# Kernel optimization log

Measured on AMD Instinct MI355X. Metric: run time of the kernel, lower is better.

The kernel has to match this reference:

```python
import jax, jax.numpy as jnp
import numpy as np

LN_EPS = 1e-5


def _ln(h, g, b):
    mu = h.mean(-1, keepdims=True)
    var = ((h - mu) ** 2).mean(-1, keepdims=True)
    return (h - mu) / jnp.sqrt(var + LN_EPS) * g + b


def setup_inputs() -> dict:
    key = jax.random.key(0)
    ks = jax.random.split(key, 12)
    B, T, Cin, C, D, M = 16, 1024, 512, 1024, 256, 1024
    s = 0.02
    inp = {
        "x": jax.random.normal(ks[0], (B, T, Cin), jnp.float32),
        "masks": jnp.ones((B, T), jnp.float32),
        "W1": jax.random.normal(ks[1], (Cin, C), jnp.float32) * s,
        "g1": jnp.ones((C,), jnp.float32), "b1": jnp.zeros((C,), jnp.float32),
        "W2": jax.random.normal(ks[2], (C, C), jnp.float32) * s,
        "g2": jnp.ones((C,), jnp.float32), "b2": jnp.zeros((C,), jnp.float32),
        "W3": jax.random.normal(ks[3], (C, C), jnp.float32) * s,
        "g3": jnp.ones((C,), jnp.float32), "b3": jnp.zeros((C,), jnp.float32),
        "W4": jax.random.normal(ks[4], (C, C), jnp.float32) * s,
        "g4": jnp.ones((C,), jnp.float32), "b4": jnp.zeros((C,), jnp.float32),
        "W5": jax.random.normal(ks[5], (C, D), jnp.float32) * s,
        "b5": jnp.zeros((D,), jnp.float32),
        # Dirichlet(alpha=100) rows, as in the torch init: rows live on the simplex
        "embedding": jax.random.dirichlet(ks[6], jnp.full((D,), 100.0, jnp.float32), (M,)).astype(jnp.float32),
    }
    return inp


def reference(x, masks, W1, g1, b1, W2, g2, b2, W3, g3, b3, W4, g4, b4, W5, b5, embedding):
    h = jax.nn.relu(_ln(x @ W1, g1, b1))
    h = jax.nn.relu(_ln(h @ W2, g2, b2))
    h = jax.nn.relu(_ln(h @ W3, g3, b3))
    h = jax.nn.relu(_ln(h @ W4, g4, b4))
    z = h @ W5 + b5                              # [B, T, D]
    p = jax.nn.log_softmax(z, axis=-1)           # log-prob features

    B, T, D = p.shape
    p_flat = jax.lax.stop_gradient(p.reshape(-1, D))   # x.detach() in torch
    ep = jnp.exp(p_flat)                               # [N, D]
    # KL(exp(p) || e_m) summed over D, for all codes m:
    #   sum_d exp(p)*(p - log(e_m)) = rowsum(exp(p)*p) - exp(p) @ log(E)^T
    div = (ep * p_flat).sum(-1, keepdims=True) - ep @ jnp.log(embedding).T  # [N, M]
    idx = jnp.argmin(div, axis=-1)                     # [N]
    quant = jax.lax.stop_gradient(embedding[idx].reshape(B, T, D))

    # commitment loss: masked KL(exp(p) || quant.detach())
    kl = (jnp.exp(p) * (p - jnp.log(quant))).sum(-1)   # [B, T]
    loss = 0.25 * (kl * masks).mean(0).sum()

    # straight-through estimator
    q = p + jax.lax.stop_gradient(quant - p)
    return z, q, loss
```

## Files before the change

### kernel.cpp

```cpp
#include <hip/hip_runtime.h>
#include <hip/hip_bf16.h>
#include <stdint.h>

typedef __attribute__((ext_vector_type(4))) float f32x4;
typedef __attribute__((ext_vector_type(8))) __bf16 bf16x8;
typedef __attribute__((ext_vector_type(4))) __bf16 bf16x4;

#define LN_EPS 1e-5f

__device__ __forceinline__ void gload_lds16(const void* g, void* l) {
  __builtin_amdgcn_global_load_lds(
      (__attribute__((address_space(1))) void*)(uintptr_t)g,
      (__attribute__((address_space(3))) void*)(uint32_t)(uintptr_t)l,
      16, 0, 0);
}

__device__ __forceinline__ f32x4 mfma16(bf16x8 a, bf16x8 b, f32x4 c) {
  return __builtin_amdgcn_mfma_f32_16x16x32_bf16(a, b, c, 0, 0, 0);
}

__global__ __launch_bounds__(256) void k_cvt_bf16(const float* __restrict__ x,
                                                  __bf16* __restrict__ o) {
  int i = (blockIdx.x * 256 + threadIdx.x) * 8;
  f32x4 a = *(const f32x4*)(x + i);
  f32x4 b = *(const f32x4*)(x + i + 4);
  bf16x8 v;
#pragma unroll
  for (int j = 0; j < 4; ++j) { v[j] = (__bf16)a[j]; v[j + 4] = (__bf16)b[j]; }
  *(bf16x8*)(o + i) = v;
}

__global__ void k_transpose(const float* __restrict__ W, __bf16* __restrict__ Wt,
                            int K, int N) {
  __shared__ float t[32][33];
  int nt = blockIdx.x * 32, kt = blockIdx.y * 32;
  int tx = threadIdx.x, ty = threadIdx.y;
  t[ty][tx] = W[(size_t)(kt + ty) * N + nt + tx];
  __syncthreads();
  Wt[(size_t)(nt + ty) * K + kt + tx] = (__bf16)t[tx][ty];
}

__global__ void k_transpose3(const float* __restrict__ Wa, const float* __restrict__ Wb,
                             const float* __restrict__ Wc, __bf16* __restrict__ Ta,
                             __bf16* __restrict__ Tb, __bf16* __restrict__ Tc) {
  __shared__ float t[32][33];
  const float* W = blockIdx.z == 0 ? Wa : (blockIdx.z == 1 ? Wb : Wc);
  __bf16* T = blockIdx.z == 0 ? Ta : (blockIdx.z == 1 ? Tb : Tc);
  int nt = blockIdx.x * 32, kt = blockIdx.y * 32;
  int tx = threadIdx.x, ty = threadIdx.y;
  t[ty][tx] = W[(size_t)(kt + ty) * 1024 + nt + tx];
  __syncthreads();
  T[(size_t)(nt + ty) * 1024 + kt + tx] = (__bf16)t[tx][ty];
}

__global__ __launch_bounds__(256) void k_logE(const float* __restrict__ e,
                                              __bf16* __restrict__ o) {
  int i = blockIdx.x * 256 + threadIdx.x;
  o[i] = (__bf16)logf(e[i] * 256.0f);
}

__global__ __launch_bounds__(512, 2) void k_gemm256(
    const __bf16* __restrict__ A, const __bf16* __restrict__ Bt,
    __bf16* __restrict__ O, int N, int K) {
  __shared__ char lds[131072];
  const int tid = threadIdx.x;
  const int lane = tid & 63;
  const int wid = tid >> 6;
  const int wm = wid >> 2;
  const int wn = wid & 3;
  const int swz = ((blockIdx.x & 7) << 5) | (blockIdx.x >> 3);
  const int bm0 = (swz & 63) * 256;
  const int bn0 = (swz >> 6) * 256;
  const int NT = K >> 6;

  const int slin = tid * 16;
  const int lrow = slin >> 7;
  const int scol = (slin & 127) ^ ((lrow & 7) << 4);
  const char* Ab = (const char*)A;
  const char* Bb = (const char*)Bt;
  const uint32_t rs = (uint32_t)K * 2;

  const int klo = (lane >> 4) * 16;
  const int sw = (lane & 7) << 4;
  const uint32_t kx0 = (uint32_t)(klo ^ sw);
  const uint32_t kx1 = (uint32_t)((64 + klo) ^ sw);
  const uint32_t abase = (uint32_t)(wm * 128 + (lane & 15)) * 128;
  const uint32_t bbase = (uint32_t)(wn * 64 + (lane & 15)) * 128;

  f32x4 acc[8][4];
#pragma unroll
  for (int i = 0; i < 8; ++i)
#pragma unroll
    for (int j = 0; j < 4; ++j) acc[i][j] = 0.0f;

#define LDSA(buf) (lds + (buf)*32768)
#define LDSB(buf) (lds + 65536 + (buf)*32768)
#define STAGE_A(t, h)                                                              \
  {                                                                                \
    const char* src = Ab + (size_t)(bm0 + (h)*128 + lrow) * rs + ((t) << 7) + scol;\
    char* dst = LDSA((t)&1) + (h)*16384 + slin;                                    \
    gload_lds16(src, dst);                                                         \
    gload_lds16(src + (size_t)64 * rs, dst + 8192);                                \
  }
#define STAGE_B(t, h)                                                              \
  {                                                                                \
    const char* src = Bb + (size_t)(bn0 + (h)*128 + lrow) * rs + ((t) << 7) + scol;\
    char* dst = LDSB((t)&1) + (h)*16384 + slin;                                    \
    gload_lds16(src, dst);                                                         \
    gload_lds16(src + (size_t)64 * rs, dst + 8192);                                \
  }

  STAGE_A(0, 0); STAGE_A(0, 1); STAGE_B(0, 0); STAGE_B(0, 1);
  STAGE_B(1, 0); STAGE_B(1, 1);
  asm volatile("s_waitcnt vmcnt(4)" ::: "memory");
  __builtin_amdgcn_s_barrier();
  asm volatile("" ::: "memory");

  for (int t = 0; t < NT; ++t) {
    const char* Acur = LDSA(t & 1);
    const char* Bcur = LDSB(t & 1);
    bf16x8 bF[4][2];
#pragma unroll
    for (int p = 0; p < 4; ++p) {
      const uint32_t ar = abase + (uint32_t)(2 * p) * 2048;
      bf16x8 a00 = *(const bf16x8*)(Acur + ar + kx0);
      bf16x8 a01 = *(const bf16x8*)(Acur + ar + kx1);
      bf16x8 a10 = *(const bf16x8*)(Acur + ar + 2048 + kx0);
      bf16x8 a11 = *(const bf16x8*)(Acur + ar + 2048 + kx1);
      if (p == 0) {
#pragma unroll
        for (int ni = 0; ni < 4; ++ni) {
          bF[ni][0] = *(const bf16x8*)(Bcur + bbase + ni * 2048 + kx0);
          bF[ni][1] = *(const bf16x8*)(Bcur + bbase + ni * 2048 + kx1);
        }
      }
      if (p == 0 && t + 1 < NT) STAGE_A(t + 1, 0);
      if (p == 1) {
        if (t + 1 < NT) STAGE_A(t + 1, 1);
        if (t + 2 < NT) STAGE_B(t + 2, 0);
      }
      if (p == 2 && t + 2 < NT) STAGE_B(t + 2, 1);

      asm volatile("" ::: "memory");
      __builtin_amdgcn_s_barrier();
      asm volatile("" ::: "memory");
      __builtin_amdgcn_s_setprio(1);
#pragma unroll
      for (int ni = 0; ni < 4; ++ni) {
        acc[2 * p][ni] = mfma16(a00, bF[ni][0], acc[2 * p][ni]);
        acc[2 * p][ni] = mfma16(a01, bF[ni][1], acc[2 * p][ni]);
        acc[2 * p + 1][ni] = mfma16(a10, bF[ni][0], acc[2 * p + 1][ni]);
        acc[2 * p + 1][ni] = mfma16(a11, bF[ni][1], acc[2 * p + 1][ni]);
      }
      __builtin_amdgcn_s_setprio(0);
      if (p == 3) asm volatile("s_waitcnt vmcnt(4)" ::: "memory");
      asm volatile("" ::: "memory");
      __builtin_amdgcn_s_barrier();
      asm volatile("" ::: "memory");
    }
  }
#undef STAGE_A
#undef STAGE_B
#undef LDSA
#undef LDSB

  const int r0 = (lane >> 4) * 4;
  const int cc = lane & 15;
#pragma unroll
  for (int mi = 0; mi < 8; ++mi) {
#pragma unroll
    for (int ni = 0; ni < 4; ++ni) {
      int r = bm0 + wm * 128 + mi * 16 + r0;
      int c = bn0 + wn * 64 + ni * 16 + cc;
#pragma unroll
      for (int j = 0; j < 4; ++j)
        O[(size_t)(r + j) * N + c] = (__bf16)acc[mi][ni][j];
    }
  }
}

__global__ __launch_bounds__(256) void k_ln_relu(__bf16* __restrict__ h,
                                                 const float* __restrict__ g,
                                                 const float* __restrict__ b) {
  int lane = threadIdx.x & 63;
  int row = blockIdx.x * 4 + (threadIdx.x >> 6);
  __bf16* rp = h + (size_t)row * 1024;
  bf16x8 v0 = *(const bf16x8*)(rp + lane * 8);
  bf16x8 v1 = *(const bf16x8*)(rp + 512 + lane * 8);
  float f0[8], f1[8];
  float s = 0.f, sq = 0.f;
#pragma unroll
  for (int j = 0; j < 8; ++j) {
    f0[j] = (float)v0[j]; f1[j] = (float)v1[j];
    s += f0[j] + f1[j];
    sq += f0[j] * f0[j] + f1[j] * f1[j];
  }
#pragma unroll
  for (int d = 1; d < 64; d <<= 1) { s += __shfl_xor(s, d); sq += __shfl_xor(sq, d); }
  float mu = s * (1.0f / 1024.0f);
  float var = sq * (1.0f / 1024.0f) - mu * mu;
  float rstd = rsqrtf(var + LN_EPS);
  const f32x4* gv = (const f32x4*)g;
  const f32x4* bv = (const f32x4*)b;
  f32x4 ga0 = gv[lane * 2], ga1 = gv[lane * 2 + 1];
  f32x4 gb0 = gv[128 + lane * 2], gb1 = gv[128 + lane * 2 + 1];
  f32x4 ba0 = bv[lane * 2], ba1 = bv[lane * 2 + 1];
  f32x4 bb0 = bv[128 + lane * 2], bb1 = bv[128 + lane * 2 + 1];
  bf16x8 o0, o1;
#pragma unroll
  for (int j = 0; j < 4; ++j) {
    float t0 = (f0[j] - mu) * rstd * ga0[j] + ba0[j];
    float t1 = (f0[j + 4] - mu) * rstd * ga1[j] + ba1[j];
    float t2 = (f1[j] - mu) * rstd * gb0[j] + bb0[j];
    float t3 = (f1[j + 4] - mu) * rstd * gb1[j] + bb1[j];
    o0[j] = (__bf16)fmaxf(t0, 0.f);
    o0[j + 4] = (__bf16)fmaxf(t1, 0.f);
    o1[j] = (__bf16)fmaxf(t2, 0.f);
    o1[j + 4] = (__bf16)fmaxf(t3, 0.f);
  }
  *(bf16x8*)(rp + lane * 8) = o0;
  *(bf16x8*)(rp + 512 + lane * 8) = o1;
}

__global__ __launch_bounds__(256) void k_gemm_sm(
    const __bf16* __restrict__ A, const __bf16* __restrict__ Bt,
    const float* __restrict__ bias, float* __restrict__ z,
    __bf16* __restrict__ ep, float* __restrict__ sm) {
  const int K = 1024;
  __shared__ char lds[40960];
  char* ldsA = lds;
  char* ldsB = lds + 8192;
  const int tid = threadIdx.x;
  const int lane = tid & 63;
  const int wn = tid >> 6;
  const int bm0 = blockIdx.x * 64;
  const char* Ab = (const char*)A;
  const char* Bb = (const char*)Bt;
  const uint32_t rs = (uint32_t)K * 2;

  const int cc = lane & 15;
  uint32_t ra[2][4], rb[2][4];
  {
    const int sww = (lane & 7) << 4;
    const int gk = lane & 48;
#pragma unroll
    for (int kk = 0; kk < 2; ++kk) {
#pragma unroll
      for (int i = 0; i < 4; ++i) {
        uint32_t kb = (uint32_t)((kk * 64 + gk) ^ sww);
        ra[kk][i] = (uint32_t)(i * 16 + cc) * 128 + kb;
        rb[kk][i] = (uint32_t)(wn * 64 + i * 16 + cc) * 128 + kb;
      }
    }
  }

  f32x4 acc[4][4];
#pragma unroll
  for (int i = 0; i < 4; ++i)
#pragma unroll
    for (int j = 0; j < 4; ++j) acc[i][j] = 0.0f;

  for (int k0 = 0; k0 < K; k0 += 64) {
    __syncthreads();
#pragma unroll
    for (int i = 0; i < 2; ++i) {
      int lin = i * 4096 + tid * 16;
      int row = lin >> 7;
      int col = (lin & 127) ^ ((row & 7) << 4);
      gload_lds16(Ab + (size_t)(bm0 + row) * rs + k0 * 2 + col, ldsA + lin);
    }
#pragma unroll
    for (int i = 0; i < 8; ++i) {
      int lin = i * 4096 + tid * 16;
      int row = lin >> 7;
      int col = (lin & 127) ^ ((row & 7) << 4);
      gload_lds16(Bb + (size_t)row * rs + k0 * 2 + col, ldsB + lin);
    }
    __syncthreads();
#pragma unroll
    for (int kk = 0; kk < 2; ++kk) {
      bf16x8 af[4], bfv[4];
#pragma unroll
      for (int i = 0; i < 4; ++i) af[i] = *(const bf16x8*)(ldsA + ra[kk][i]);
#pragma unroll
      for (int i = 0; i < 4; ++i) bfv[i] = *(const bf16x8*)(ldsB + rb[kk][i]);
#pragma unroll
      for (int mi = 0; mi < 4; ++mi)
#pragma unroll
        for (int ni = 0; ni < 4; ++ni)
          acc[mi][ni] = mfma16(af[mi], bfv[ni], acc[mi][ni]);
    }
  }

  __syncthreads();
  float* stm = (float*)lds;
  float* sts = (float*)(lds + 1024);
  float* rowm = (float*)(lds + 2048);
  float* rows_ = (float*)(lds + 2304);

  const int r0 = (lane >> 4) * 4;
  float bvv[4];
#pragma unroll
  for (int ni = 0; ni < 4; ++ni) bvv[ni] = bias[wn * 64 + ni * 16 + cc];

  float zv[4][4];
#pragma unroll
  for (int mi = 0; mi < 4; ++mi) {
#pragma unroll
    for (int j = 0; j < 4; ++j) {
      float m = -3.4e38f;
#pragma unroll
      for (int ni = 0; ni < 4; ++ni) {
        zv[mi][ni] = acc[mi][ni][j] + bvv[ni];
        m = fmaxf(m, zv[mi][ni]);
      }
#pragma unroll
      for (int d = 1; d < 16; d <<= 1) m = fmaxf(m, __shfl_xor(m, d));
      if (cc == 0) stm[wn * 64 + mi * 16 + r0 + j] = m;
    }
  }
  __syncthreads();
  if (tid < 64) {
    float m = fmaxf(fmaxf(stm[tid], stm[64 + tid]), fmaxf(stm[128 + tid], stm[192 + tid]));
    rowm[tid] = m;
  }
  __syncthreads();
#pragma unroll
  for (int mi = 0; mi < 4; ++mi) {
#pragma unroll
    for (int j = 0; j < 4; ++j) {
      int r = mi * 16 + r0 + j;
      float m = rowm[r];
      float s = 0.f;
#pragma unroll
      for (int ni = 0; ni < 4; ++ni) s += expf(acc[mi][ni][j] + bvv[ni] - m);
#pragma unroll
      for (int d = 1; d < 16; d <<= 1) s += __shfl_xor(s, d);
      if (cc == 0) sts[wn * 64 + r] = s;
    }
  }
  __syncthreads();
  if (tid < 64) {
    float s = sts[tid] + sts[64 + tid] + sts[128 + tid] + sts[192 + tid];
    rows_[tid] = s;
    sm[bm0 + tid] = rowm[tid] + logf(s);
  }
  __syncthreads();
#pragma unroll
  for (int mi = 0; mi < 4; ++mi) {
#pragma unroll
    for (int j = 0; j < 4; ++j) {
      int r = mi * 16 + r0 + j;
      float m = rowm[r];
      float inv = 1.0f / rows_[r];
      float* zp = z + (size_t)(bm0 + r) * 256;
      __bf16* epp = ep + (size_t)(bm0 + r) * 256;
#pragma unroll
      for (int ni = 0; ni < 4; ++ni) {
        int c = wn * 64 + ni * 16 + cc;
        float zz = acc[mi][ni][j] + bvv[ni];
        zp[c] = zz;
        epp[c] = (__bf16)(expf(zz - m) * inv);
      }
    }
  }
}

__global__ __launch_bounds__(256) void k_gemm_div(
    const __bf16* __restrict__ A, const __bf16* __restrict__ Bt,
    float* __restrict__ part_val, int* __restrict__ part_idx, int N, int K) {
  __shared__ char lds[32768];
  char* ldsA = lds;
  char* ldsB = lds + 16384;
  const int tid = threadIdx.x;
  const int lane = tid & 63;
  const int wid = tid >> 6;
  const int wm = wid >> 1, wn = wid & 1;
  const int bm0 = blockIdx.x * 128;
  const int bn0 = blockIdx.y * 128;

  const int slin = tid * 16;
  const int srow = slin >> 7;
  const int scol = (slin & 127) ^ ((srow & 7) << 4);

  const char* Ab = (const char*)A;
  const char* Bb = (const char*)Bt;
  const uint32_t rs = (uint32_t)K * 2;

  uint32_t ra[2][4], rb[2][4];
  {
    const int sw = (lane & 7) << 4;
    const int gk = lane & 48;
#pragma unroll
    for (int kk = 0; kk < 2; ++kk) {
#pragma unroll
      for (int i = 0; i < 4; ++i) {
        uint32_t kb = (uint32_t)((kk * 64 + gk) ^ sw);
        ra[kk][i] = (uint32_t)(wm * 64 + i * 16 + (lane & 15)) * 128 + kb;
        rb[kk][i] = (uint32_t)(wn * 64 + i * 16 + (lane & 15)) * 128 + kb;
      }
    }
  }

  f32x4 acc[4][4];
#pragma unroll
  for (int i = 0; i < 4; ++i)
#pragma unroll
    for (int j = 0; j < 4; ++j) acc[i][j] = 0.0f;

  for (int k0 = 0; k0 < K; k0 += 64) {
    __syncthreads();
    const uint32_t kbyte = (uint32_t)k0 * 2 + (uint32_t)scol;
#pragma unroll
    for (int i = 0; i < 4; ++i) {
      int row = i * 32 + srow;
      gload_lds16(Ab + (size_t)(bm0 + row) * rs + kbyte, ldsA + i * 4096 + slin);
    }
#pragma unroll
    for (int i = 0; i < 4; ++i) {
      int row = i * 32 + srow;
      gload_lds16(Bb + (size_t)(bn0 + row) * rs + kbyte, ldsB + i * 4096 + slin);
    }
    __syncthreads();
#pragma unroll
    for (int kk = 0; kk < 2; ++kk) {
      bf16x8 af[4], bfv[4];
#pragma unroll
      for (int i = 0; i < 4; ++i) af[i] = *(const bf16x8*)(ldsA + ra[kk][i]);
#pragma unroll
      for (int i = 0; i < 4; ++i) bfv[i] = *(const bf16x8*)(ldsB + rb[kk][i]);
#pragma unroll
      for (int mi = 0; mi < 4; ++mi)
#pragma unroll
        for (int ni = 0; ni < 4; ++ni)
          acc[mi][ni] = mfma16(af[mi], bfv[ni], acc[mi][ni]);
    }
  }

  const int r0 = (lane >> 4) * 4;
  const int cc = lane & 15;
  const int nch = N >> 6;
#pragma unroll
  for (int mi = 0; mi < 4; ++mi) {
#pragma unroll
    for (int j = 0; j < 4; ++j) {
      float v = acc[mi][0][j];
      int c = cc;
#pragma unroll
      for (int ni = 1; ni < 4; ++ni) {
        float v2 = acc[mi][ni][j];
        int c2 = ni * 16 + cc;
        if (v2 > v) { v = v2; c = c2; }
      }
#pragma unroll
      for (int d = 1; d < 16; d <<= 1) {
        float ov = __shfl_xor(v, d);
        int oc = __shfl_xor(c, d);
        if (ov > v || (ov == v && oc < c)) { v = ov; c = oc; }
      }
      if (cc == 0) {
        int r = bm0 + wm * 64 + mi * 16 + r0 + j;
        int chunk = (bn0 >> 6) + wn;
        part_val[r * nch + chunk] = v;
        part_idx[r * nch + chunk] = bn0 + wn * 64 + c;
      }
    }
  }
}

__global__ __launch_bounds__(256) void k_final(
    const float* __restrict__ part_val, const int* __restrict__ part_idx,
    const float* __restrict__ z, const float* __restrict__ sm,
    const float* __restrict__ emb, const float* __restrict__ masks,
    float* __restrict__ q, float* __restrict__ blockloss) {
  __shared__ float ls[4];
  int lane = threadIdx.x & 63;
  int w = threadIdx.x >> 6;
  int row = blockIdx.x * 4 + w;
  float v = -3.4e38f;
  int c = 0x7fffffff;
  if (lane < 16) { v = part_val[row * 16 + lane]; c = part_idx[row * 16 + lane]; }
#pragma unroll
  for (int d = 1; d < 16; d <<= 1) {
    float ov = __shfl_xor(v, d);
    int oc = __shfl_xor(c, d);
    if (ov > v || (ov == v && oc < c)) { v = ov; c = oc; }
  }
  int code = __shfl(c, 0);
  f32x4 ev = ((const f32x4*)(emb + (size_t)code * 256))[lane];
  ((f32x4*)(q + (size_t)row * 256))[lane] = ev;
  f32x4 zv = ((const f32x4*)(z + (size_t)row * 256))[lane];
  float smr = sm[row];
  float kl = 0.f;
#pragma unroll
  for (int j = 0; j < 4; ++j) {
    float pj = zv[j] - smr;
    kl += expf(pj) * (pj - logf(ev[j]));
  }
#pragma unroll
  for (int d = 1; d < 64; d <<= 1) kl += __shfl_xor(kl, d);
  if (lane == 0) ls[w] = kl * masks[row];
  __syncthreads();
  if (threadIdx.x == 0) blockloss[blockIdx.x] = ls[0] + ls[1] + ls[2] + ls[3];
}

__global__ __launch_bounds__(256) void k_loss_reduce(const float* __restrict__ bl,
                                                     float* __restrict__ out) {
  __shared__ float s[256];
  float a = 0.f;
#pragma unroll
  for (int i = 0; i < 16; ++i) a += bl[threadIdx.x + i * 256];
  s[threadIdx.x] = a;
  __syncthreads();
  for (int st = 128; st > 0; st >>= 1) {
    if (threadIdx.x < st) s[threadIdx.x] += s[threadIdx.x + st];
    __syncthreads();
  }
  if (threadIdx.x == 0) out[0] = s[0] * (0.25f / 16.0f);
}

extern "C" void kernel_launch(void* const* d_in, const int* in_sizes, int n_in,
                              void* d_out, int out_size, void* d_ws, size_t ws_size,
                              hipStream_t stream) {
  const float* x = (const float*)d_in[0];
  const float* masks = (const float*)d_in[1];
  const float* W1 = (const float*)d_in[2];
  const float* g1 = (const float*)d_in[3];
  const float* b1 = (const float*)d_in[4];
  const float* W2 = (const float*)d_in[5];
  const float* g2 = (const float*)d_in[6];
  const float* b2 = (const float*)d_in[7];
  const float* W3 = (const float*)d_in[8];
  const float* g3 = (const float*)d_in[9];
  const float* b3 = (const float*)d_in[10];
  const float* W4 = (const float*)d_in[11];
  const float* g4 = (const float*)d_in[12];
  const float* b4 = (const float*)d_in[13];
  const float* W5 = (const float*)d_in[14];
  const float* b5 = (const float*)d_in[15];
  const float* emb = (const float*)d_in[16];

  const int M = 16384;
  char* ws = (char*)d_ws;
  __bf16* bufA = (__bf16*)(ws);
  __bf16* bufB = (__bf16*)(ws + (32ull << 20));
  __bf16* W1t = (__bf16*)(ws + (64ull << 20));
  __bf16* W2t = (__bf16*)(ws + (65ull << 20));
  __bf16* W3t = (__bf16*)(ws + (67ull << 20));
  __bf16* W4t = (__bf16*)(ws + (69ull << 20));
  __bf16* W5t = (__bf16*)(ws + (71ull << 20));
  __bf16* logE = (__bf16*)(ws + (72ull << 20));
  float* part_val = (float*)(ws + (73ull << 20));
  int* part_idx = (int*)(ws + (74ull << 20));
  float* blockloss = (float*)(ws + (75ull << 20));
  float* sm = (float*)(ws + (76ull << 20));
  __bf16* ep = (__bf16*)(ws + (16ull << 20));

  float* z = (float*)d_out;
  float* q = z + (size_t)M * 256;
  float* lossp = z + 2ull * M * 256;

  dim3 tb32(32, 32);
  k_cvt_bf16<<<4096, 256, 0, stream>>>(x, bufB);
  k_transpose<<<dim3(32, 16), tb32, 0, stream>>>(W1, W1t, 512, 1024);
  k_transpose3<<<dim3(32, 32, 3), tb32, 0, stream>>>(W2, W3, W4, W2t, W3t, W4t);
  k_transpose<<<dim3(8, 32), tb32, 0, stream>>>(W5, W5t, 1024, 256);
  k_logE<<<1024, 256, 0, stream>>>(emb, logE);

  k_gemm256<<<256, 512, 0, stream>>>(bufB, W1t, bufA, 1024, 512);
  k_ln_relu<<<4096, 256, 0, stream>>>(bufA, g1, b1);
  k_gemm256<<<256, 512, 0, stream>>>(bufA, W2t, bufB, 1024, 1024);
  k_ln_relu<<<4096, 256, 0, stream>>>(bufB, g2, b2);
  k_gemm256<<<256, 512, 0, stream>>>(bufB, W3t, bufA, 1024, 1024);
  k_ln_relu<<<4096, 256, 0, stream>>>(bufA, g3, b3);
  k_gemm256<<<256, 512, 0, stream>>>(bufA, W4t, bufB, 1024, 1024);
  k_ln_relu<<<4096, 256, 0, stream>>>(bufB, g4, b4);
  k_gemm_sm<<<256, 256, 0, stream>>>(bufB, W5t, b5, z, ep, sm);
  k_gemm_div<<<dim3(128, 8), 256, 0, stream>>>(ep, logE, part_val, part_idx, 1024, 256);
  k_final<<<4096, 256, 0, stream>>>(part_val, part_idx, z, sm, emb, masks, q, blockloss);
  k_loss_reduce<<<1, 256, 0, stream>>>(blockloss, lossp);
}
```

Before: 281.4 us.

## Restructure GEMM main loop into two half-phases and drop block swizzle

Rewrites the k_gemm256 inner loop from four quarter-phases with a barrier around each into two half-phases. Each half loads A fragments for four M-subtiles and runs 32 MFMAs, with sched_barriers replacing memory clobbers. Global-to-LDS staging is regrouped: all of next A at loop start, all of B two tiles ahead after the mid barrier. It also replaces the XCD-aware block swizzle with a plain 2D grid, which may change L2 locality across XCDs, and drops a temporary array in the softmax epilogue.

```diff
diff --git a/kernel.cpp b/kernel.cpp
--- a/kernel.cpp
+++ b/kernel.cpp
@@ -68,9 +68,8 @@
   const int wid = tid >> 6;
   const int wm = wid >> 2;
   const int wn = wid & 3;
-  const int swz = ((blockIdx.x & 7) << 5) | (blockIdx.x >> 3);
-  const int bm0 = (swz & 63) * 256;
-  const int bn0 = (swz >> 6) * 256;
+  const int bm0 = blockIdx.x * 256;
+  const int bn0 = blockIdx.y * 256;
   const int NT = K >> 6;
 
   const int slin = tid * 16;
@@ -112,51 +111,63 @@
 
   STAGE_A(0, 0); STAGE_A(0, 1); STAGE_B(0, 0); STAGE_B(0, 1);
   STAGE_B(1, 0); STAGE_B(1, 1);
-  asm volatile("s_waitcnt vmcnt(4)" ::: "memory");
+  asm volatile("s_waitcnt vmcnt(4)");
   __builtin_amdgcn_s_barrier();
-  asm volatile("" ::: "memory");
+  __builtin_amdgcn_sched_barrier(0);
 
   for (int t = 0; t < NT; ++t) {
     const char* Acur = LDSA(t & 1);
     const char* Bcur = LDSB(t & 1);
+
+    if (t + 1 < NT) { STAGE_A(t + 1, 0); STAGE_A(t + 1, 1); }
     bf16x8 bF[4][2];
 #pragma unroll
-    for (int p = 0; p < 4; ++p) {
-      const uint32_t ar = abase + (uint32_t)(2 * p) * 2048;
-      bf16x8 a00 = *(const bf16x8*)(Acur + ar + kx0);
-      bf16x8 a01 = *(const bf16x8*)(Acur + ar + kx1);
-      bf16x8 a10 = *(const bf16x8*)(Acur + ar + 2048 + kx0);
-      bf16x8 a11 = *(const bf16x8*)(Acur + ar + 2048 + kx1);
-      if (p == 0) {
+    for (int ni = 0; ni < 4; ++ni) {
+      bF[ni][0] = *(const bf16x8*)(Bcur + bbase + ni * 2048 + kx0);
+      bF[ni][1] = *(const bf16x8*)(Bcur + bbase + ni * 2048 + kx1);
+    }
+    {
+      bf16x8 aF[4][2];
+#pragma unroll
+      for (int mi = 0; mi < 4; ++mi) {
+        aF[mi][0] = *(const bf16x8*)(Acur + abase + mi * 2048 + kx0);
+        aF[mi][1] = *(const bf16x8*)(Acur + abase + mi * 2048 + kx1);
+      }
+      __builtin_amdgcn_s_setprio(1);
+#pragma unroll
+      for (int mi = 0; mi < 4; ++mi)
 #pragma unroll
         for (int ni = 0; ni < 4; ++ni) {
-          bF[ni][0] = *(const bf16x8*)(Bcur + bbase + ni * 2048 + kx0);
-          bF[ni][1] = *(const bf16x8*)(Bcur + bbase + ni * 2048 + kx1);
+          acc[mi][ni] = mfma16(aF[mi][0], bF[ni][0], acc[mi][ni]);
+          acc[mi][ni] = mfma16(aF[mi][1], bF[ni][1], acc[mi][ni]);
         }
-      }
-      if (p == 0 && t + 1 < NT) STAGE_A(t + 1, 0);
-      if (p == 1) {
-        if (t + 1 < NT) STAGE_A(t + 1, 1);
-        if (t + 2 < NT) STAGE_B(t + 2, 0);
-      }
-      if (p == 2 && t + 2 < NT) STAGE_B(t + 2, 1);
-
-      asm volatile("" ::: "memory");
+      __builtin_amdgcn_s_setprio(0);
+    }
+    __builtin_amdgcn_s_barrier();
+    __builtin_amdgcn_sched_barrier(0);
+
+    if (t + 2 < NT) { STAGE_B(t + 2, 0); STAGE_B(t + 2, 1); }
+    {
+      bf16x8 aF[4][2];
+#pragma unroll
+      for (int mi = 0; mi < 4; ++mi) {
+        aF[mi][0] = *(const bf16x8*)(Acur + abase + (mi + 4) * 2048 + kx0);
+        aF[mi][1] = *(const bf16x8*)(Acur + abase + (mi + 4) * 2048 + kx1);
+      }
+      __builtin_amdgcn_s_setprio(1);
+#pragma unroll
+      for (int mi = 0; mi < 4; ++mi)
+#pragma unroll
+        for (int ni = 0; ni < 4; ++ni) {
+          acc[mi + 4][ni] = mfma16(aF[mi][0], bF[ni][0], acc[mi + 4][ni]);
+          acc[mi + 4][ni] = mfma16(aF[mi][1], bF[ni][1], acc[mi + 4][ni]);
+        }
+      __builtin_amdgcn_s_setprio(0);
+    }
+    if (t + 1 < NT) {
+      asm volatile("s_waitcnt vmcnt(4)");
       __builtin_amdgcn_s_barrier();
-      asm volatile("" ::: "memory");
-      __builtin_amdgcn_s_setprio(1);
-#pragma unroll
-      for (int ni = 0; ni < 4; ++ni) {
-        acc[2 * p][ni] = mfma16(a00, bF[ni][0], acc[2 * p][ni]);
-        acc[2 * p][ni] = mfma16(a01, bF[ni][1], acc[2 * p][ni]);
-        acc[2 * p + 1][ni] = mfma16(a10, bF[ni][0], acc[2 * p + 1][ni]);
-        acc[2 * p + 1][ni] = mfma16(a11, bF[ni][1], acc[2 * p + 1][ni]);
-      }
-      __builtin_amdgcn_s_setprio(0);
-      if (p == 3) asm volatile("s_waitcnt vmcnt(4)" ::: "memory");
-      asm volatile("" ::: "memory");
-      __builtin_amdgcn_s_barrier();
-      asm volatile("" ::: "memory");
+      __builtin_amdgcn_sched_barrier(0);
     }
   }
 #undef STAGE_A
@@ -303,17 +314,13 @@
 #pragma unroll
   for (int ni = 0; ni < 4; ++ni) bvv[ni] = bias[wn * 64 + ni * 16 + cc];
 
-  float zv[4][4];
 #pragma unroll
   for (int mi = 0; mi < 4; ++mi) {
 #pragma unroll
     for (int j = 0; j < 4; ++j) {
       float m = -3.4e38f;
 #pragma unroll
-      for (int ni = 0; ni < 4; ++ni) {
-        zv[mi][ni] = acc[mi][ni][j] + bvv[ni];
-        m = fmaxf(m, zv[mi][ni]);
-      }
+      for (int ni = 0; ni < 4; ++ni) m = fmaxf(m, acc[mi][ni][j] + bvv[ni]);
 #pragma unroll
       for (int d = 1; d < 16; d <<= 1) m = fmaxf(m, __shfl_xor(m, d));
       if (cc == 0) stm[wn * 64 + mi * 16 + r0 + j] = m;
@@ -567,13 +574,13 @@
   k_transpose<<<dim3(8, 32), tb32, 0, stream>>>(W5, W5t, 1024, 256);
   k_logE<<<1024, 256, 0, stream>>>(emb, logE);
 
-  k_gemm256<<<256, 512, 0, stream>>>(bufB, W1t, bufA, 1024, 512);
+  k_gemm256<<<dim3(64, 4), 512, 0, stream>>>(bufB, W1t, bufA, 1024, 512);
   k_ln_relu<<<4096, 256, 0, stream>>>(bufA, g1, b1);
-  k_gemm256<<<256, 512, 0, stream>>>(bufA, W2t, bufB, 1024, 1024);
+  k_gemm256<<<dim3(64, 4), 512, 0, stream>>>(bufA, W2t, bufB, 1024, 1024);
   k_ln_relu<<<4096, 256, 0, stream>>>(bufB, g2, b2);
-  k_gemm256<<<256, 512, 0, stream>>>(bufB, W3t, bufA, 1024, 1024);
+  k_gemm256<<<dim3(64, 4), 512, 0, stream>>>(bufB, W3t, bufA, 1024, 1024);
   k_ln_relu<<<4096, 256, 0, stream>>>(bufA, g3, b3);
-  k_gemm256<<<256, 512, 0, stream>>>(bufA, W4t, bufB, 1024, 1024);
+  k_gemm256<<<dim3(64, 4), 512, 0, stream>>>(bufA, W4t, bufB, 1024, 1024);
   k_ln_relu<<<4096, 256, 0, stream>>>(bufB, g4, b4);
   k_gemm_sm<<<256, 256, 0, stream>>>(bufB, W5t, b5, z, ep, sm);
   k_gemm_div<<<dim3(128, 8), 256, 0, stream>>>(ep, logE, part_val, part_idx, 1024, 256);
```

Result: faster. 271.0 us (-3.7%).
